# Optimization experiments

Hardware: AMD Instinct MI355X
Metric: run time of the kernel (lower is better)

## Reference

```python
import jax, jax.numpy as jnp
import numpy as np

NUM_HEADS = 16
HEAD_DIM = 80  # embed_dim 1280 / 16


def setup_inputs() -> dict:
    key = jax.random.key(0)
    ks = jax.random.split(key, 5)
    E = NUM_HEADS * HEAD_DIM
    sq, b = 1024, 8
    x = jax.random.normal(ks[0], (sq, b, E), dtype=jnp.float32)
    w_in = jax.random.normal(ks[1], (E, 3 * E), dtype=jnp.float32) * (E ** -0.5)
    b_in = jax.random.normal(ks[2], (3 * E,), dtype=jnp.float32) * 0.01
    w_out = jax.random.normal(ks[3], (E, E), dtype=jnp.float32) * (E ** -0.5)
    b_out = jax.random.normal(ks[4], (E,), dtype=jnp.float32) * 0.01
    return {"x": x, "w_in": w_in, "b_in": b_in, "w_out": w_out, "b_out": b_out}


def reference(x, w_in, b_in, w_out, b_out):
    sq, b, E = x.shape
    H, D = NUM_HEADS, HEAD_DIM
    norm_factor = jnp.asarray(D ** 0.5, x.dtype)
    # in_proj: [sq, b, 3E] -> [sq, b, H, 3D], split into q/k/v along last dim
    mixed = (x @ w_in + b_in).reshape(sq, b, H, 3 * D)
    q, k, v = jnp.split(mixed, 3, axis=-1)  # each [sq, b, H, D]
    # merge (b, H) and move to batch-of-bmm layout [b*H, sq, D]
    q = q.reshape(sq, b * H, D).transpose(1, 0, 2) / norm_factor
    k = k.reshape(sq, b * H, D).transpose(1, 0, 2)
    v = v.reshape(sq, b * H, D).transpose(1, 0, 2)
    scores = jnp.einsum('nqd,nkd->nqk', q, k)  # [b*H, sq, sq]
    probs = jax.nn.softmax(scores, axis=-1)
    ctx = jnp.einsum('nqk,nkd->nqd', probs, v)  # [b*H, sq, D]
    # [b, H, sq, D] -> [sq, b, H, D] -> [sq, b, E]
    ctx = ctx.reshape(b, H, sq, D).transpose(2, 0, 1, 3).reshape(sq, b, E)
    return ctx @ w_out + b_out
```

## Files before the change

kernel.cpp:

```cpp
#include <hip/hip_runtime.h>

#define DEVI __device__ __forceinline__

typedef _Float16 f16x8 __attribute__((ext_vector_type(8)));
typedef _Float16 f16x4v __attribute__((ext_vector_type(4)));
typedef _Float16 f16x2 __attribute__((ext_vector_type(2)));
typedef __fp16 fp16x2 __attribute__((ext_vector_type(2)));
typedef float f32x4 __attribute__((ext_vector_type(4)));
typedef float f32x16 __attribute__((ext_vector_type(16)));
typedef unsigned u32x4 __attribute__((ext_vector_type(4)));

DEVI void gl16(const void* g, void* l) {
  __builtin_amdgcn_global_load_lds((const __attribute__((address_space(1))) void*)g,
                                   (__attribute__((address_space(3))) void*)l, 16, 0, 0);
}

#define VMCNT(N) asm volatile("s_waitcnt vmcnt(" #N ")" ::: "memory")
#define LGKM0() asm volatile("s_waitcnt lgkmcnt(0)" ::: "memory")
#define BARRIER() asm volatile("s_barrier" ::: "memory")

DEVI unsigned pk2(float a, float b) {
  fp16x2 t = __builtin_amdgcn_cvt_pkrtz(a, b);
  return __builtin_bit_cast(unsigned, t);
}
DEVI void pl32swap(unsigned &a, unsigned &b) {
  asm volatile("v_permlane32_swap_b32 %0, %1" : "+v"(a), "+v"(b));
}

__global__ __launch_bounds__(256) void k_cvt(const float* __restrict__ in, _Float16* __restrict__ out, int n4) {
  int i = blockIdx.x * 256 + threadIdx.x;
  int stride = gridDim.x * 256;
  for (; i < n4; i += stride) {
    float4 v = ((const float4*)in)[i];
    f16x4v h = { (_Float16)v.x, (_Float16)v.y, (_Float16)v.z, (_Float16)v.w };
    ((f16x4v*)out)[i] = h;
  }
}

__global__ __launch_bounds__(256) void k_transpose(const float* __restrict__ in, _Float16* __restrict__ out,
                                                   int R, int C) {
  __shared__ float t[32][33];
  int cb = blockIdx.x * 32, rb = blockIdx.y * 32;
  int tx = threadIdx.x & 31, ty = threadIdx.x >> 5;
  #pragma unroll
  for (int i = ty; i < 32; i += 8) t[i][tx] = in[(size_t)(rb + i) * C + cb + tx];
  __syncthreads();
  #pragma unroll
  for (int i = ty; i < 32; i += 8) out[(size_t)(cb + i) * R + rb + tx] = (_Float16)t[tx][i];
}


#define MM(NLO, AF, BF) do {                                                                       \
    __builtin_amdgcn_s_setprio(1);                                                                 \
    _Pragma("unroll")                                                                              \
    for (int m_ = 0; m_ < 8; m_++) {                                                               \
      acc[m_][NLO]     = __builtin_amdgcn_mfma_f32_16x16x32_f16(AF[m_], BF[NLO],     acc[m_][NLO],     0, 0, 0); \
      acc[m_][NLO + 1] = __builtin_amdgcn_mfma_f32_16x16x32_f16(AF[m_], BF[NLO + 1], acc[m_][NLO + 1], 0, 0, 0); \
    }                                                                                              \
    __builtin_amdgcn_s_setprio(0);                                                                 \
  } while (0)

#define LDA(KT, KK, DST) do {                                                                      \
    const _Float16* bas_ = &smem[(size_t)((((KT) & 1) * 2) + wr) * 8192];                          \
    _Pragma("unroll")                                                                              \
    for (int m_ = 0; m_ < 8; m_++)                                                                 \
      DST[m_] = *(const f16x8*)&bas_[(m_ * 16 + ln) * 64 + (((((KK) * 4) + g) ^ chB) << 3)];       \
  } while (0)

#define LDB(KT, KK, DST) do {                                                                      \
    const _Float16* bas_ = &smem[32768 + (size_t)((((KT) & 1) * 2) + (wc >> 1)) * 8192];           \
    _Pragma("unroll")                                                                              \
    for (int n_ = 0; n_ < 4; n_++)                                                                 \
      DST[n_] = *(const f16x8*)&bas_[((wc & 1) * 64 + n_ * 16 + ln) * 64 + (((((KK) * 4) + g) ^ chB) << 3)]; \
  } while (0)

template<int M, int N, int K>
__global__ __launch_bounds__(512, 2) void k_gemm8(const _Float16* __restrict__ A, const _Float16* __restrict__ BT,
                                                  const float* __restrict__ bias,
                                                  _Float16* __restrict__ qo, _Float16* __restrict__ ko,
                                                  _Float16* __restrict__ vo) {
  extern __shared__ _Float16 smem[];
  constexpr int NT = K / 64;
  constexpr int NI = NT / 2;
  const int tid = threadIdx.x;
  const int w = tid >> 6, lane = tid & 63, ln = lane & 15, g = lane >> 4;
  const int wr = w >> 2, wc = w & 3;
  const int l8 = lane >> 3, l7 = lane & 7;
  const int stChunk = (l7 ^ l8) << 3;
  const int chB = ln & 7;

  constexpr int MT = M / 256;
  const int xcd = blockIdx.x & 7;
  const int i = blockIdx.x >> 3;
  const int bm0 = (xcd * (MT / 8) + (i & 3)) * 256;
  const int bn0 = (i >> 2) * 256;

  auto stgA = [&](int kt, int hh) {
    _Float16* ldsb = &smem[(size_t)((kt & 1) * 2 + hh) * 8192 + w * 1024];
    const _Float16* g0 = &A[(size_t)(bm0 + hh * 128 + w * 16 + l8) * K + kt * 64 + stChunk];
    gl16(g0, ldsb);
    gl16(g0 + (size_t)8 * K, ldsb + 512);
  };
  auto stgB = [&](int kt, int hh) {
    _Float16* ldsb = &smem[32768 + (size_t)((kt & 1) * 2 + hh) * 8192 + w * 1024];
    const _Float16* g0 = &BT[(size_t)(bn0 + hh * 128 + w * 16 + l8) * K + kt * 64 + stChunk];
    gl16(g0, ldsb);
    gl16(g0 + (size_t)8 * K, ldsb + 512);
  };

  f32x4 acc[8][4] = {};
  f16x8 a0[8], a1[8], b0[4], b1[4];

  stgB(0, 0); stgB(0, 1); stgA(0, 0); stgA(0, 1);
  stgB(1, 0); stgB(1, 1); stgA(1, 0);
  VMCNT(6);
  BARRIER();
  LDA(0, 0, a0); LDB(0, 0, b0);

  for (int it = 0; it < NI; ++it) {
    const int T0 = 2 * it, T1 = 2 * it + 1;
    const int S0 = (T0 + 2 < NT) ? T0 + 2 : 0;
    const int S1 = (T1 + 2 < NT) ? T1 + 2 : 1;
    LDB(T0, 1, b1);
    stgA(T1, 1);
    BARRIER();
    MM(0, a0, b0);
    LGKM0(); BARRIER();
    LDA(T0, 1, a1);
    stgB(S0, 0);
    BARRIER();
    MM(2, a0, b0);
    LGKM0(); BARRIER();
    stgB(S0, 1);
    BARRIER();
    MM(0, a1, b1);
    VMCNT(4);
    LGKM0(); BARRIER();
    LDA(T1, 0, a0); LDB(T1, 0, b0);
    stgA(S0, 0);
    BARRIER();
    MM(2, a1, b1);
    LGKM0(); BARRIER();
    LDB(T1, 1, b1);
    stgA(S0, 1);
    BARRIER();
    MM(0, a0, b0);
    LGKM0(); BARRIER();
    LDA(T1, 1, a1);
    stgB(S1, 0);
    BARRIER();
    MM(2, a0, b0);
    LGKM0(); BARRIER();
    stgB(S1, 1);
    BARRIER();
    MM(0, a1, b1);
    VMCNT(4);
    LGKM0(); BARRIER();
    LDA(S0, 0, a0); LDB(S0, 0, b0);
    stgA(S1, 0);
    BARRIER();
    MM(2, a1, b1);
    LGKM0(); BARRIER();
  }

  VMCNT(0);
  BARRIER();
  _Float16* sH = smem;
  #pragma unroll
  for (int n = 0; n < 4; n++) {
    int col = wc * 64 + n * 16 + ln;
    int gcol = bn0 + col;
    float bv = bias[gcol];
    int hq = gcol / 240;
    int tt = gcol - hq * 240;
    float scl = (tt < 80) ? (0.11180339887498948f * 1.4426950408889634f) : 1.0f;
    #pragma unroll
    for (int m = 0; m < 8; m++) {
      #pragma unroll
      for (int r = 0; r < 4; r++) {
        int row = wr * 128 + m * 16 + 4 * g + r;
        sH[row * 256 + col] = (_Float16)((acc[m][n][r] + bv) * scl);
      }
    }
  }
  LGKM0();
  BARRIER();
  #pragma unroll
  for (int i2 = 0; i2 < 16; i2++) {
    int id = tid + 512 * i2;
    int row = id >> 5, c8 = id & 31;
    f16x8 v = *(const f16x8*)&sH[row * 256 + c8 * 8];
    int gcol = bn0 + c8 * 8;
    int grow = bm0 + row;
    int hq = gcol / 240;
    int tt = gcol - hq * 240;
    int reg = tt / 80;
    int cc = tt - reg * 80;
    int s = grow >> 3;
    int head = (grow & 7) * 16 + hq;
    _Float16* dst = (reg == 0) ? qo : (reg == 1) ? ko : vo;
    *(f16x8*)&dst[(size_t)(head * 1024 + s) * 80 + cc] = v;
  }
}

template<int M, int N, int K>
__global__ __launch_bounds__(256) void k_gemm(const _Float16* __restrict__ A, const _Float16* __restrict__ BT,
                                              const float* __restrict__ bias, float* __restrict__ outF) {
  __shared__ _Float16 Al[128 * 32];
  __shared__ _Float16 Bl[128 * 32];
  const int tid = threadIdx.x;
  const int w = tid >> 6, lane = tid & 63, ln = lane & 15, g = lane >> 4;
  const int bm0 = blockIdx.x * 128, bn0 = blockIdx.y * 128;
  const int wm = (w >> 1) * 64, wn = (w & 1) * 64;
  const int r0 = tid >> 2, c0 = (tid & 3) * 8;
  f32x4 acc[4][4] = {};
  for (int kt = 0; kt < K; kt += 32) {
    __syncthreads();
    gl16(&A[(size_t)(bm0 + r0) * K + kt + c0],      &Al[(w * 64) * 8]);
    gl16(&A[(size_t)(bm0 + r0 + 64) * K + kt + c0], &Al[(256 + w * 64) * 8]);
    gl16(&BT[(size_t)(bn0 + r0) * K + kt + c0],      &Bl[(w * 64) * 8]);
    gl16(&BT[(size_t)(bn0 + r0 + 64) * K + kt + c0], &Bl[(256 + w * 64) * 8]);
    __syncthreads();
    f16x8 af[4], bf[4];
    #pragma unroll
    for (int i = 0; i < 4; i++) af[i] = *(const f16x8*)&Al[(wm + i * 16 + ln) * 32 + g * 8];
    #pragma unroll
    for (int i = 0; i < 4; i++) bf[i] = *(const f16x8*)&Bl[(wn + i * 16 + ln) * 32 + g * 8];
    #pragma unroll
    for (int i = 0; i < 4; i++)
      #pragma unroll
      for (int j = 0; j < 4; j++)
        acc[i][j] = __builtin_amdgcn_mfma_f32_16x16x32_f16(af[i], bf[j], acc[i][j], 0, 0, 0);
  }
  #pragma unroll
  for (int j = 0; j < 4; j++) {
    int col = bn0 + wn + j * 16 + ln;
    float bv = bias[col];
    #pragma unroll
    for (int i = 0; i < 4; i++) {
      int mb = bm0 + wm + i * 16 + 4 * g;
      #pragma unroll
      for (int r = 0; r < 4; r++)
        outF[(size_t)(mb + r) * N + col] = acc[i][j][r] + bv;
    }
  }
}

__global__ __launch_bounds__(256) void k_vtrans(const _Float16* __restrict__ vb, _Float16* __restrict__ vT) {
  __shared__ _Float16 t[64][81];
  int head = blockIdx.x >> 4;
  int sb = (blockIdx.x & 15) * 64;
  for (int idx = threadIdx.x; idx < 64 * 80; idx += 256) {
    int s = idx / 80, d = idx - s * 80;
    t[s][d] = vb[(head * 1024 + sb + s) * 80 + d];
  }
  __syncthreads();
  for (int idx = threadIdx.x; idx < 80 * 64; idx += 256) {
    int d = idx >> 6, s = idx & 63;
    vT[(head * 80 + d) * 1024 + sb + s] = t[s][d];
  }
}

__global__ __launch_bounds__(512, 2) void k_attn(const _Float16* __restrict__ qb, const _Float16* __restrict__ kb,
                                                 const _Float16* __restrict__ vT, _Float16* __restrict__ ctxg) {
  extern __shared__ _Float16 smem[];
  _Float16* Kb0 = smem;
  _Float16* Kb1 = smem + 8192;
  _Float16* Vb0 = smem + 16384;
  _Float16* Vb1 = smem + 16384 + 6144;

  const int tid = threadIdx.x;
  const int w = tid >> 6, lane = tid & 63;
  const int l32 = lane & 31, h = lane >> 5;
  const int lx = l32 & 7;
  const int xcd = blockIdx.x & 7;
  const int j = blockIdx.x >> 3;
  const int head = xcd + 8 * (j & 15);
  const int s0 = (j >> 4) * 256;
  const int bb = head >> 4, h16 = head & 15;

  const int c1 = (tid < 128) ? tid + 512 : tid;
  const int kr0 = tid / 10, kh0 = tid - kr0 * 10;
  const int kr1 = c1 / 10,  kh1 = c1 - kr1 * 10;
  const int vr0 = tid >> 3, vh0 = tid & 7;
  const int vr1 = c1 >> 3,  vh1 = c1 & 7;
  const int kO0 = kr0 * 128 + ((kh0 ^ (kr0 & 7)) << 3);
  const int kO1 = kr1 * 128 + ((kh1 ^ (kr1 & 7)) << 3);
  const int vO0 = vr0 * 64 + ((vh0 ^ (vr0 & 7)) << 3);
  const int vO1 = vr1 * 64 + ((vh1 ^ (vr1 & 7)) << 3);
  const _Float16* kG0 = kb + (size_t)head * 81920 + kr0 * 80 + kh0 * 8;
  const _Float16* kG1 = kb + (size_t)head * 81920 + kr1 * 80 + kh1 * 8;
  const _Float16* vG0 = vT + (size_t)head * 81920 + vr0 * 1024 + vh0 * 8;
  const _Float16* vG1 = vT + (size_t)head * 81920 + vr1 * 1024 + vh1 * 8;

  uint4 krA, krB, vrA, vrB;
  auto issue = [&](int kt) {
    krA = *(const uint4*)(kG0 + kt * 5120);
    krB = *(const uint4*)(kG1 + kt * 5120);
    vrA = *(const uint4*)(vG0 + kt * 64);
    vrB = *(const uint4*)(vG1 + kt * 64);
  };
  auto stage = [&](int b) {
    _Float16* kd = b ? Kb1 : Kb0;
    _Float16* vd = b ? Vb1 : Vb0;
    *(uint4*)(kd + kO0) = krA;
    *(uint4*)(kd + kO1) = krB;
    *(uint4*)(vd + vO0) = vrA;
    *(uint4*)(vd + vO1) = vrB;
  };

  const int qrow = s0 + w * 32 + l32;
  f16x8 qf[5];
  #pragma unroll
  for (int s = 0; s < 5; s++)
    qf[s] = *(const f16x8*)&qb[(size_t)(head * 1024 + qrow) * 80 + s * 16 + h * 8];

  f32x16 ct[3] = {};
  float m_run = -INFINITY, l_run = 0.f;

  issue(0);
  stage(0);
  LGKM0();
  BARRIER();
  issue(1);

  for (int kt = 0; kt < 16; ++kt) {
    const _Float16* kc = (kt & 1) ? Kb1 : Kb0;
    const _Float16* vc = (kt & 1) ? Vb1 : Vb0;

    f32x16 sc0 = {}, sc1 = {};
    __builtin_amdgcn_s_setprio(1);
    #pragma unroll
    for (int s = 0; s < 5; ++s) {
      f16x8 kf0 = *(const f16x8*)&kc[l32 * 128 + (((2 * s + h) ^ lx) << 3)];
      f16x8 kf1 = *(const f16x8*)&kc[(32 + l32) * 128 + (((2 * s + h) ^ lx) << 3)];
      sc0 = __builtin_amdgcn_mfma_f32_32x32x16_f16(kf0, qf[s], sc0, 0, 0, 0);
      sc1 = __builtin_amdgcn_mfma_f32_32x32x16_f16(kf1, qf[s], sc1, 0, 0, 0);
    }
    __builtin_amdgcn_s_setprio(0);

    float mx[8];
    #pragma unroll
    for (int i = 0; i < 8; ++i)
      mx[i] = fmaxf(fmaxf(sc0[i], sc0[i + 8]), fmaxf(sc1[i], sc1[i + 8]));
    #pragma unroll
    for (int i = 0; i < 4; ++i) mx[i] = fmaxf(mx[i], mx[i + 4]);
    float tm = fmaxf(fmaxf(mx[0], mx[2]), fmaxf(mx[1], mx[3]));
    tm = fmaxf(tm, __shfl_xor(tm, 32));
    float mnew = fmaxf(m_run, tm);
    float fac = exp2f(m_run - mnew);
    float p0[16], p1[16];
    #pragma unroll
    for (int i = 0; i < 16; ++i) p0[i] = exp2f(sc0[i] - mnew);
    #pragma unroll
    for (int i = 0; i < 16; ++i) p1[i] = exp2f(sc1[i] - mnew);
    float ps = 0.f;
    #pragma unroll
    for (int i = 0; i < 16; ++i) ps += p0[i] + p1[i];

    unsigned fr[4][4];
    #define PACK4(T, PP) do {                                                \
        _Pragma("unroll")                                                    \
        for (int s16 = 0; s16 < 2; ++s16) {                                  \
          unsigned u0 = pk2(PP[8 * s16 + 0], PP[8 * s16 + 1]);               \
          unsigned u1 = pk2(PP[8 * s16 + 2], PP[8 * s16 + 3]);               \
          unsigned u2 = pk2(PP[8 * s16 + 4], PP[8 * s16 + 5]);               \
          unsigned u3 = pk2(PP[8 * s16 + 6], PP[8 * s16 + 7]);               \
          pl32swap(u0, u2); pl32swap(u1, u3);                                \
          fr[2 * (T) + s16][0] = u0; fr[2 * (T) + s16][1] = u1;              \
          fr[2 * (T) + s16][2] = u2; fr[2 * (T) + s16][3] = u3;              \
        }                                                                    \
      } while (0)
    PACK4(0, p0);
    PACK4(1, p1);

    l_run = l_run * fac + (ps + __shfl_xor(ps, 32));
    m_run = mnew;

    #pragma unroll
    for (int dt = 0; dt < 3; ++dt)
      #pragma unroll
      for (int i = 0; i < 16; ++i) ct[dt][i] *= fac;

    __builtin_amdgcn_s_setprio(1);
    #pragma unroll
    for (int ss = 0; ss < 4; ++ss) {
      u32x4 fu = { fr[ss][0], fr[ss][1], fr[ss][2], fr[ss][3] };
      f16x8 pf = __builtin_bit_cast(f16x8, fu);
      #pragma unroll
      for (int dt = 0; dt < 3; ++dt) {
        f16x8 vf = *(const f16x8*)&vc[(dt * 32 + l32) * 64 + (((2 * ss + h) ^ lx) << 3)];
        ct[dt] = __builtin_amdgcn_mfma_f32_32x32x16_f16(vf, pf, ct[dt], 0, 0, 0);
      }
    }
    __builtin_amdgcn_s_setprio(0);

    if (kt < 15) {
      stage((kt + 1) & 1);
      LGKM0();
      BARRIER();
      if (kt < 14) issue(kt + 2);
    }
  }

  float inv = 1.f / l_run;
  int sq = s0 + w * 32 + l32;
  _Float16* outp = ctxg + (size_t)(sq * 8 + bb) * 1280 + h16 * 80 + 4 * h;
  #pragma unroll
  for (int dt = 0; dt < 3; ++dt)
    #pragma unroll
    for (int rq = 0; rq < 4; ++rq) {
      if (dt == 2 && rq >= 2) continue;
      f16x4v o = { (_Float16)(ct[dt][rq * 4 + 0] * inv), (_Float16)(ct[dt][rq * 4 + 1] * inv),
                   (_Float16)(ct[dt][rq * 4 + 2] * inv), (_Float16)(ct[dt][rq * 4 + 3] * inv) };
      *(f16x4v*)&outp[dt * 32 + rq * 8] = o;
    }
}

extern "C" void kernel_launch(void* const* d_in, const int* in_sizes, int n_in,
                              void* d_out, int out_size, void* d_ws, size_t ws_size,
                              hipStream_t stream) {
  const float* x     = (const float*)d_in[0];
  const float* w_in  = (const float*)d_in[1];
  const float* b_in  = (const float*)d_in[2];
  const float* w_out = (const float*)d_in[3];
  const float* b_out = (const float*)d_in[4];
  float* out = (float*)d_out;

  char* ws = (char*)d_ws;
  size_t off = 0;
  auto carve = [&](size_t bytes) -> void* {
    void* p = ws + off;
    off += (bytes + 255) & ~(size_t)255;
    return p;
  };
  _Float16* xb     = (_Float16*)carve(8192ull * 1280 * 2);
  _Float16* w_inT  = (_Float16*)carve(3840ull * 1280 * 2);
  _Float16* w_outT = (_Float16*)carve(1280ull * 1280 * 2);
  _Float16* qb     = (_Float16*)carve(128ull * 1024 * 80 * 2);
  _Float16* kbuf   = (_Float16*)carve(128ull * 1024 * 80 * 2);
  _Float16* vb     = (_Float16*)carve(128ull * 1024 * 80 * 2);
  _Float16* vT     = (_Float16*)carve(128ull * 1024 * 80 * 2);
  _Float16* ctxg   = (_Float16*)carve(8192ull * 1280 * 2);
  if (off > ws_size) return;

  hipFuncSetAttribute(reinterpret_cast<const void*>(&k_gemm8<8192, 3840, 1280>),
                      hipFuncAttributeMaxDynamicSharedMemorySize, 131072);
  hipFuncSetAttribute(reinterpret_cast<const void*>(&k_attn),
                      hipFuncAttributeMaxDynamicSharedMemorySize, 57344);

  k_cvt<<<2048, 256, 0, stream>>>(x, xb, 8192 * 1280 / 4);
  k_transpose<<<dim3(120, 40), 256, 0, stream>>>(w_in, w_inT, 1280, 3840);
  k_transpose<<<dim3(40, 40), 256, 0, stream>>>(w_out, w_outT, 1280, 1280);

  k_gemm8<8192, 3840, 1280><<<480, 512, 131072, stream>>>(xb, w_inT, b_in, qb, kbuf, vb);
  k_vtrans<<<2048, 256, 0, stream>>>(vb, vT);
  k_attn<<<512, 512, 57344, stream>>>(qb, kbuf, vT, ctxg);
  k_gemm<8192, 1280, 1280><<<dim3(64, 10), 256, 0, stream>>>(ctxg, w_outT, b_out, out);
}
```

Baseline: 255.7 us.

## Fuse prep kernels into one launch and triple-buffer B tiles in QKV GEMM

Merges the fp32→fp16 conversion of x and the two weight transposes into a single k_prep launch, dispatched by block index, to cut launch overhead and the gaps between kernels. The in-projection GEMM now keeps three LDS slots for B tiles instead of two and issues its loads a stage earlier, with the vmcnt waits relaxed to match. This raises dynamic LDS per block from 128 KB to 160 KB, which may stop two blocks from fitting on one CU despite launch_bounds(512,2).

```diff
diff --git a/kernel.cpp b/kernel.cpp
--- a/kernel.cpp
+++ b/kernel.cpp
@@ -27,21 +27,27 @@
   asm volatile("v_permlane32_swap_b32 %0, %1" : "+v"(a), "+v"(b));
 }
 
-__global__ __launch_bounds__(256) void k_cvt(const float* __restrict__ in, _Float16* __restrict__ out, int n4) {
-  int i = blockIdx.x * 256 + threadIdx.x;
-  int stride = gridDim.x * 256;
-  for (; i < n4; i += stride) {
-    float4 v = ((const float4*)in)[i];
-    f16x4v h = { (_Float16)v.x, (_Float16)v.y, (_Float16)v.z, (_Float16)v.w };
-    ((f16x4v*)out)[i] = h;
-  }
-}
-
-__global__ __launch_bounds__(256) void k_transpose(const float* __restrict__ in, _Float16* __restrict__ out,
-                                                   int R, int C) {
+__global__ __launch_bounds__(256) void k_prep(const float* __restrict__ x, _Float16* __restrict__ xb,
+                                              const float* __restrict__ w_in, _Float16* __restrict__ w_inT,
+                                              const float* __restrict__ w_out, _Float16* __restrict__ w_outT) {
   __shared__ float t[32][33];
-  int cb = blockIdx.x * 32, rb = blockIdx.y * 32;
-  int tx = threadIdx.x & 31, ty = threadIdx.x >> 5;
+  int bid = blockIdx.x;
+  int tid = threadIdx.x;
+  if (bid < 2048) {
+    const int n4 = 8192 * 1280 / 4;
+    for (int i = bid * 256 + tid; i < n4; i += 2048 * 256) {
+      float4 v = ((const float4*)x)[i];
+      f16x4v h = { (_Float16)v.x, (_Float16)v.y, (_Float16)v.z, (_Float16)v.w };
+      ((f16x4v*)xb)[i] = h;
+    }
+    return;
+  }
+  const float* in; _Float16* out; int R, C, tIdx;
+  if (bid < 6848) { in = w_in;  out = w_inT;  R = 1280; C = 3840; tIdx = bid - 2048; }
+  else            { in = w_out; out = w_outT; R = 1280; C = 1280; tIdx = bid - 6848; }
+  int ntc = C / 32;
+  int cb = (tIdx % ntc) * 32, rb = (tIdx / ntc) * 32;
+  int tx = tid & 31, ty = tid >> 5;
   #pragma unroll
   for (int i = ty; i < 32; i += 8) t[i][tx] = in[(size_t)(rb + i) * C + cb + tx];
   __syncthreads();
@@ -67,8 +73,8 @@
       DST[m_] = *(const f16x8*)&bas_[(m_ * 16 + ln) * 64 + (((((KK) * 4) + g) ^ chB) << 3)];       \
   } while (0)
 
-#define LDB(KT, KK, DST) do {                                                                      \
-    const _Float16* bas_ = &smem[32768 + (size_t)((((KT) & 1) * 2) + (wc >> 1)) * 8192];           \
+#define LDB(SLOT, KK, DST) do {                                                                    \
+    const _Float16* bas_ = &smem[32768 + (size_t)(SLOT) * 16384 + (size_t)(wc >> 1) * 8192];       \
     _Pragma("unroll")                                                                              \
     for (int n_ = 0; n_ < 4; n_++)                                                                 \
       DST[n_] = *(const f16x8*)&bas_[((wc & 1) * 64 + n_ * 16 + ln) * 64 + (((((KK) * 4) + g) ^ chB) << 3)]; \
@@ -101,8 +107,8 @@
     gl16(g0, ldsb);
     gl16(g0 + (size_t)8 * K, ldsb + 512);
   };
-  auto stgB = [&](int kt, int hh) {
-    _Float16* ldsb = &smem[32768 + (size_t)((kt & 1) * 2 + hh) * 8192 + w * 1024];
+  auto stgB = [&](int slot, int kt, int hh) {
+    _Float16* ldsb = &smem[32768 + (size_t)slot * 16384 + (size_t)hh * 8192 + w * 1024];
     const _Float16* g0 = &BT[(size_t)(bn0 + hh * 128 + w * 16 + l8) * K + kt * 64 + stChunk];
     gl16(g0, ldsb);
     gl16(g0 + (size_t)8 * K, ldsb + 512);
@@ -111,56 +117,42 @@
   f32x4 acc[8][4] = {};
   f16x8 a0[8], a1[8], b0[4], b1[4];
 
-  stgB(0, 0); stgB(0, 1); stgA(0, 0); stgA(0, 1);
-  stgB(1, 0); stgB(1, 1); stgA(1, 0);
-  VMCNT(6);
+  stgB(0, 0, 0); stgB(0, 0, 1); stgB(1, 1, 0); stgB(1, 1, 1);
+  stgA(0, 0); stgA(0, 1); stgA(1, 0); stgA(1, 1);
+  VMCNT(4);
   BARRIER();
   LDA(0, 0, a0); LDB(0, 0, b0);
 
   for (int it = 0; it < NI; ++it) {
     const int T0 = 2 * it, T1 = 2 * it + 1;
-    const int S0 = (T0 + 2 < NT) ? T0 + 2 : 0;
-    const int S1 = (T1 + 2 < NT) ? T1 + 2 : 1;
-    LDB(T0, 1, b1);
-    stgA(T1, 1);
-    BARRIER();
-    MM(0, a0, b0);
-    LGKM0(); BARRIER();
+    const int S0w = (T0 + 2 < NT) ? T0 + 2 : 0;
+    const int S1w = (T1 + 2 < NT) ? T1 + 2 : 1;
+    const int sT0 = T0 % 3;
+    const int sT1 = (sT0 + 1 == 3) ? 0 : sT0 + 1;
+    const int sS0 = (sT1 + 1 == 3) ? 0 : sT1 + 1;
+    const int sS1 = sT0;
+    LDB(sT0, 1, b1);
+    stgB(sS0, S0w, 0);
+    BARRIER(); MM(0, a0, b0); LGKM0(); BARRIER();
     LDA(T0, 1, a1);
-    stgB(S0, 0);
-    BARRIER();
-    MM(2, a0, b0);
-    LGKM0(); BARRIER();
-    stgB(S0, 1);
-    BARRIER();
-    MM(0, a1, b1);
-    VMCNT(4);
-    LGKM0(); BARRIER();
-    LDA(T1, 0, a0); LDB(T1, 0, b0);
-    stgA(S0, 0);
-    BARRIER();
-    MM(2, a1, b1);
-    LGKM0(); BARRIER();
-    LDB(T1, 1, b1);
-    stgA(S0, 1);
-    BARRIER();
-    MM(0, a0, b0);
-    LGKM0(); BARRIER();
+    stgB(sS0, S0w, 1);
+    BARRIER(); MM(2, a0, b0); LGKM0(); BARRIER();
+    stgA(S0w, 0);
+    BARRIER(); MM(0, a1, b1); VMCNT(6); LGKM0(); BARRIER();
+    LDA(T1, 0, a0); LDB(sT1, 0, b0);
+    stgA(S0w, 1);
+    BARRIER(); MM(2, a1, b1); LGKM0(); BARRIER();
+    LDB(sT1, 1, b1);
+    stgB(sS1, S1w, 0);
+    BARRIER(); MM(0, a0, b0); LGKM0(); BARRIER();
     LDA(T1, 1, a1);
-    stgB(S1, 0);
-    BARRIER();
-    MM(2, a0, b0);
-    LGKM0(); BARRIER();
-    stgB(S1, 1);
-    BARRIER();
-    MM(0, a1, b1);
-    VMCNT(4);
-    LGKM0(); BARRIER();
-    LDA(S0, 0, a0); LDB(S0, 0, b0);
-    stgA(S1, 0);
-    BARRIER();
-    MM(2, a1, b1);
-    LGKM0(); BARRIER();
+    stgB(sS1, S1w, 1);
+    BARRIER(); MM(2, a0, b0); LGKM0(); BARRIER();
+    stgA(S1w, 0);
+    BARRIER(); MM(0, a1, b1); VMCNT(6); LGKM0(); BARRIER();
+    LDA(S0w, 0, a0); LDB(sS0, 0, b0);
+    stgA(S1w, 1);
+    BARRIER(); MM(2, a1, b1); LGKM0(); BARRIER();
   }
 
   VMCNT(0);
@@ -445,15 +437,13 @@
   if (off > ws_size) return;
 
   hipFuncSetAttribute(reinterpret_cast<const void*>(&k_gemm8<8192, 3840, 1280>),
-                      hipFuncAttributeMaxDynamicSharedMemorySize, 131072);
+                      hipFuncAttributeMaxDynamicSharedMemorySize, 163840);
   hipFuncSetAttribute(reinterpret_cast<const void*>(&k_attn),
                       hipFuncAttributeMaxDynamicSharedMemorySize, 57344);
 
-  k_cvt<<<2048, 256, 0, stream>>>(x, xb, 8192 * 1280 / 4);
-  k_transpose<<<dim3(120, 40), 256, 0, stream>>>(w_in, w_inT, 1280, 3840);
-  k_transpose<<<dim3(40, 40), 256, 0, stream>>>(w_out, w_outT, 1280, 1280);
-
-  k_gemm8<8192, 3840, 1280><<<480, 512, 131072, stream>>>(xb, w_inT, b_in, qb, kbuf, vb);
+  k_prep<<<8448, 256, 0, stream>>>(x, xb, w_in, w_inT, w_out, w_outT);
+
+  k_gemm8<8192, 3840, 1280><<<480, 512, 163840, stream>>>(xb, w_inT, b_in, qb, kbuf, vb);
   k_vtrans<<<2048, 256, 0, stream>>>(vb, vT);
   k_attn<<<512, 512, 57344, stream>>>(qb, kbuf, vT, ctxg);
   k_gemm<8192, 1280, 1280><<<dim3(64, 10), 256, 0, stream>>>(ctxg, w_outT, b_out, out);
```

Result: no change. 257.2 us (+0.6%).

## Fuse prep kernels, write V transposed from QKV GEMM, lazy softmax rescale

Applied to the files above, without the earlier changes.

The three conversion and transpose kernels are merged into one launch. The w_in columns are permuted so each GEMM tile holds only Q, K or V, which lets V tiles be written directly in transposed layout and removes the separate V-transpose kernel and its buffer. The attention loop now rescales the accumulator and running sum only when some lane's new max exceeds the running max by more than 8 (in log2 units), which skips most rescale multiplies. In exchange, the lazy rescale lets exponents grow up to 2^8 before rescaling, which adds some fp16 overflow or precision risk in P, and the V epilogue uses strided LDS gathers.

```diff
diff --git a/kernel.cpp b/kernel.cpp
--- a/kernel.cpp
+++ b/kernel.cpp
@@ -27,26 +27,40 @@
   asm volatile("v_permlane32_swap_b32 %0, %1" : "+v"(a), "+v"(b));
 }
 
-__global__ __launch_bounds__(256) void k_cvt(const float* __restrict__ in, _Float16* __restrict__ out, int n4) {
-  int i = blockIdx.x * 256 + threadIdx.x;
-  int stride = gridDim.x * 256;
-  for (; i < n4; i += stride) {
-    float4 v = ((const float4*)in)[i];
-    f16x4v h = { (_Float16)v.x, (_Float16)v.y, (_Float16)v.z, (_Float16)v.w };
-    ((f16x4v*)out)[i] = h;
-  }
-}
-
-__global__ __launch_bounds__(256) void k_transpose(const float* __restrict__ in, _Float16* __restrict__ out,
-                                                   int R, int C) {
+__global__ __launch_bounds__(256) void k_prep(const float* __restrict__ x, _Float16* __restrict__ xb,
+                                              const float* __restrict__ w_in, _Float16* __restrict__ w_inT,
+                                              const float* __restrict__ w_out, _Float16* __restrict__ w_outT) {
   __shared__ float t[32][33];
-  int cb = blockIdx.x * 32, rb = blockIdx.y * 32;
-  int tx = threadIdx.x & 31, ty = threadIdx.x >> 5;
+  int bid = blockIdx.x;
+  int tid = threadIdx.x;
+  if (bid < 2048) {
+    const int n4 = 8192 * 1280 / 4;
+    for (int i = bid * 256 + tid; i < n4; i += 2048 * 256) {
+      float4 v = ((const float4*)x)[i];
+      f16x4v h = { (_Float16)v.x, (_Float16)v.y, (_Float16)v.z, (_Float16)v.w };
+      ((f16x4v*)xb)[i] = h;
+    }
+    return;
+  }
+  const float* in; _Float16* out; int R, C, tIdx; bool perm;
+  if (bid < 6848) { in = w_in;  out = w_inT;  R = 1280; C = 3840; tIdx = bid - 2048; perm = true; }
+  else            { in = w_out; out = w_outT; R = 1280; C = 1280; tIdx = bid - 6848; perm = false; }
+  int ntc = C / 32;
+  int cb = (tIdx % ntc) * 32, rb = (tIdx / ntc) * 32;
+  int tx = tid & 31, ty = tid >> 5;
   #pragma unroll
   for (int i = ty; i < 32; i += 8) t[i][tx] = in[(size_t)(rb + i) * C + cb + tx];
   __syncthreads();
   #pragma unroll
-  for (int i = ty; i < 32; i += 8) out[(size_t)(cb + i) * R + rb + tx] = (_Float16)t[tx][i];
+  for (int i = ty; i < 32; i += 8) {
+    int c = cb + i;
+    if (perm) {
+      int hq = c / 240, tt = c - hq * 240;
+      int reg = tt / 80, d = tt - reg * 80;
+      c = reg * 1280 + hq * 80 + d;
+    }
+    out[(size_t)c * R + rb + tx] = (_Float16)t[tx][i];
+  }
 }
 
 
@@ -166,14 +180,14 @@
   VMCNT(0);
   BARRIER();
   _Float16* sH = smem;
+  const int regn = bn0 / 1280;
   #pragma unroll
   for (int n = 0; n < 4; n++) {
     int col = wc * 64 + n * 16 + ln;
-    int gcol = bn0 + col;
-    float bv = bias[gcol];
-    int hq = gcol / 240;
-    int tt = gcol - hq * 240;
-    float scl = (tt < 80) ? (0.11180339887498948f * 1.4426950408889634f) : 1.0f;
+    int rel = bn0 - regn * 1280 + col;
+    int h = rel / 80, d = rel - h * 80;
+    float bv = bias[h * 240 + regn * 80 + d];
+    float scl = (regn == 0) ? (0.11180339887498948f * 1.4426950408889634f) : 1.0f;
     #pragma unroll
     for (int m = 0; m < 8; m++) {
       #pragma unroll
@@ -185,21 +199,32 @@
   }
   LGKM0();
   BARRIER();
-  #pragma unroll
-  for (int i2 = 0; i2 < 16; i2++) {
-    int id = tid + 512 * i2;
-    int row = id >> 5, c8 = id & 31;
-    f16x8 v = *(const f16x8*)&sH[row * 256 + c8 * 8];
-    int gcol = bn0 + c8 * 8;
-    int grow = bm0 + row;
-    int hq = gcol / 240;
-    int tt = gcol - hq * 240;
-    int reg = tt / 80;
-    int cc = tt - reg * 80;
-    int s = grow >> 3;
-    int head = (grow & 7) * 16 + hq;
-    _Float16* dst = (reg == 0) ? qo : (reg == 1) ? ko : vo;
-    *(f16x8*)&dst[(size_t)(head * 1024 + s) * 80 + cc] = v;
+  if (regn < 2) {
+    _Float16* dst = regn ? ko : qo;
+    #pragma unroll
+    for (int i2 = 0; i2 < 16; i2++) {
+      int id = tid + 512 * i2;
+      int row = id >> 5, c8 = id & 31;
+      f16x8 v = *(const f16x8*)&sH[row * 256 + c8 * 8];
+      int rel = bn0 - regn * 1280 + c8 * 8;
+      int h = rel / 80, d0 = rel - h * 80;
+      int grow = bm0 + row;
+      *(f16x8*)&dst[(size_t)(((grow & 7) * 16 + h) * 1024 + (grow >> 3)) * 80 + d0] = v;
+    }
+  } else {
+    #pragma unroll
+    for (int t = 0; t < 16; t++) {
+      int id = tid + 512 * t;
+      int col = id & 255, rest = id >> 8;
+      int hb = rest & 7, sch = rest >> 3;
+      int rel = bn0 - 2560 + col;
+      int h = rel / 80, d = rel - h * 80;
+      f16x8 v;
+      #pragma unroll
+      for (int k = 0; k < 8; k++)
+        v[k] = sH[(hb + 8 * (sch * 8 + k)) * 256 + col];
+      *(f16x8*)&vo[(size_t)((hb * 16 + h) * 80 + d) * 1024 + (bm0 >> 3) + sch * 8] = v;
+    }
   }
 }
 
@@ -246,21 +271,6 @@
   }
 }
 
-__global__ __launch_bounds__(256) void k_vtrans(const _Float16* __restrict__ vb, _Float16* __restrict__ vT) {
-  __shared__ _Float16 t[64][81];
-  int head = blockIdx.x >> 4;
-  int sb = (blockIdx.x & 15) * 64;
-  for (int idx = threadIdx.x; idx < 64 * 80; idx += 256) {
-    int s = idx / 80, d = idx - s * 80;
-    t[s][d] = vb[(head * 1024 + sb + s) * 80 + d];
-  }
-  __syncthreads();
-  for (int idx = threadIdx.x; idx < 80 * 64; idx += 256) {
-    int d = idx >> 6, s = idx & 63;
-    vT[(head * 80 + d) * 1024 + sb + s] = t[s][d];
-  }
-}
-
 __global__ __launch_bounds__(512, 2) void k_attn(const _Float16* __restrict__ qb, const _Float16* __restrict__ kb,
                                                  const _Float16* __restrict__ vT, _Float16* __restrict__ ctxg) {
   extern __shared__ _Float16 smem[];
@@ -347,13 +357,23 @@
     for (int i = 0; i < 4; ++i) mx[i] = fmaxf(mx[i], mx[i + 4]);
     float tm = fmaxf(fmaxf(mx[0], mx[2]), fmaxf(mx[1], mx[3]));
     tm = fmaxf(tm, __shfl_xor(tm, 32));
-    float mnew = fmaxf(m_run, tm);
-    float fac = exp2f(m_run - mnew);
+
+    if (__any(tm > m_run + 8.f)) {
+      float mnew = fmaxf(m_run, tm);
+      float fac = exp2f(m_run - mnew);
+      #pragma unroll
+      for (int dt = 0; dt < 3; ++dt)
+        #pragma unroll
+        for (int i = 0; i < 16; ++i) ct[dt][i] *= fac;
+      l_run *= fac;
+      m_run = mnew;
+    }
+
     float p0[16], p1[16];
     #pragma unroll
-    for (int i = 0; i < 16; ++i) p0[i] = exp2f(sc0[i] - mnew);
-    #pragma unroll
-    for (int i = 0; i < 16; ++i) p1[i] = exp2f(sc1[i] - mnew);
+    for (int i = 0; i < 16; ++i) p0[i] = exp2f(sc0[i] - m_run);
+    #pragma unroll
+    for (int i = 0; i < 16; ++i) p1[i] = exp2f(sc1[i] - m_run);
     float ps = 0.f;
     #pragma unroll
     for (int i = 0; i < 16; ++i) ps += p0[i] + p1[i];
@@ -374,13 +394,7 @@
     PACK4(0, p0);
     PACK4(1, p1);
 
-    l_run = l_run * fac + (ps + __shfl_xor(ps, 32));
-    m_run = mnew;
-
-    #pragma unroll
-    for (int dt = 0; dt < 3; ++dt)
-      #pragma unroll
-      for (int i = 0; i < 16; ++i) ct[dt][i] *= fac;
+    l_run += ps + __shfl_xor(ps, 32);
 
     __builtin_amdgcn_s_setprio(1);
     #pragma unroll
@@ -439,7 +453,6 @@
   _Float16* w_outT = (_Float16*)carve(1280ull * 1280 * 2);
   _Float16* qb     = (_Float16*)carve(128ull * 1024 * 80 * 2);
   _Float16* kbuf   = (_Float16*)carve(128ull * 1024 * 80 * 2);
-  _Float16* vb     = (_Float16*)carve(128ull * 1024 * 80 * 2);
   _Float16* vT     = (_Float16*)carve(128ull * 1024 * 80 * 2);
   _Float16* ctxg   = (_Float16*)carve(8192ull * 1280 * 2);
   if (off > ws_size) return;
@@ -449,12 +462,9 @@
   hipFuncSetAttribute(reinterpret_cast<const void*>(&k_attn),
                       hipFuncAttributeMaxDynamicSharedMemorySize, 57344);
 
-  k_cvt<<<2048, 256, 0, stream>>>(x, xb, 8192 * 1280 / 4);
-  k_transpose<<<dim3(120, 40), 256, 0, stream>>>(w_in, w_inT, 1280, 3840);
-  k_transpose<<<dim3(40, 40), 256, 0, stream>>>(w_out, w_outT, 1280, 1280);
-
-  k_gemm8<8192, 3840, 1280><<<480, 512, 131072, stream>>>(xb, w_inT, b_in, qb, kbuf, vb);
-  k_vtrans<<<2048, 256, 0, stream>>>(vb, vT);
+  k_prep<<<8448, 256, 0, stream>>>(x, xb, w_in, w_inT, w_out, w_outT);
+
+  k_gemm8<8192, 3840, 1280><<<480, 512, 131072, stream>>>(xb, w_inT, b_in, qb, kbuf, vT);
   k_attn<<<512, 512, 57344, stream>>>(qb, kbuf, vT, ctxg);
   k_gemm<8192, 1280, 1280><<<dim3(64, 10), 256, 0, stream>>>(ctxg, w_outT, b_out, out);
 }
```

Measured after the change: 240.1 us. -6.1%, faster.
